# Kernel optimization log

Measured on AMD Instinct MI355X. Metric: run time of the kernel, lower is better.

Reference implementation:

```python
import jax, jax.numpy as jnp
import numpy as np

B_SZ, IN_DIM, N_NEURONS, N_LAYERS, N_OUTS = 65536, 4, 512, 8, 4


def setup_inputs() -> dict:
    key = jax.random.key(0)
    ks = jax.random.split(key, 5)
    glorot = lambda k, shape: jax.random.normal(k, shape, jnp.float32) * np.sqrt(2.0 / (shape[-2] + shape[-1]))
    inputs = jax.random.normal(ks[0], (B_SZ, IN_DIM), jnp.float32)
    # GaussianRFF projection matrix (fixed random Gaussian)
    B_rff = jax.random.normal(ks[1], (IN_DIM, N_NEURONS // 2), jnp.float32)
    Ws = glorot(ks[2], (N_LAYERS, N_NEURONS, N_NEURONS))
    bs = jnp.zeros((N_LAYERS, N_NEURONS), jnp.float32)
    alphas = jnp.zeros((N_LAYERS + 1,), jnp.float32)  # LAAF slopes, init 0
    Wf = glorot(ks[3], (N_NEURONS, N_OUTS))           # final mixer, no bias
    scale = jnp.ones((N_OUTS,), jnp.float32)          # Scaler, no bias
    return {"inputs": inputs, "B_rff": B_rff, "Ws": Ws, "bs": bs,
            "alphas": alphas, "Wf": Wf, "scale": scale}


def _mlp(x, B_rff, Ws, bs, alphas, Wf, scale):
    # Gaussian random Fourier feature embedding -> [B, n_neurons]
    z = x @ B_rff
    u = jnp.concatenate([jnp.sin(z), jnp.cos(z)], axis=-1)
    L = Ws.shape[0]
    def step(u, p):
        W, b, a = p
        # LAAF sine layer: sin(w0 * (1 + alpha) * (uW + b)), w0 = 1.0
        return jnp.sin((1.0 + a) * (u @ W + b)), None
    u, _ = jax.lax.scan(step, u, (Ws, bs, alphas[:L]))
    return (u @ Wf) * scale  # [B, 4] = (A1, A2, A3, phi)


def reference(inputs, B_rff, Ws, bs, alphas, Wf, scale):
    f = lambda x: _mlp(x, B_rff, Ws, bs, alphas, Wf, scale)
    def jvp_col(col):
        tang = jnp.zeros_like(inputs).at[:, col].set(1.0)
        return jax.jvp(f, (inputs,), (tang,))
    # input columns: 0=t, 1=z, 2=x, 3=y
    P, dPdz = jvp_col(1)
    _, dPdx = jvp_col(2)
    _, dPdy = jvp_col(3)
    A1_y, A1_z = dPdy[:, 0:1], dPdz[:, 0:1]
    A2_x, A2_z = dPdx[:, 1:2], dPdz[:, 1:2]
    A3_x, A3_y = dPdx[:, 2:3], dPdy[:, 2:3]
    phi_x, phi_y, phi_z = dPdx[:, 3:4], dPdy[:, 3:4], dPdz[:, 3:4]
    u = (A3_y - A2_z) + phi_x
    v = (A1_z - A3_x) + phi_y
    w = (A2_x - A1_y) + phi_z
    return jnp.concatenate([u, v, w], axis=1)
```

## Files before the change

### kernel.cpp

```cpp
#include <hip/hip_runtime.h>
#include <stdint.h>


#define B_SZ   65536
#define NN     512
#define NL     8
#define SPB    24
#define MROWS  96
#define MT     6
#define NTW    4
#define NKB    16
#define KB_BYTES 32768
#define LDS_A  (MROWS*1024)
#define LDS_TOTAL (LDS_A + 2*KB_BYTES)

typedef _Float16 f16x8 __attribute__((ext_vector_type(8)));
typedef float    f32x4 __attribute__((ext_vector_type(4)));

__device__ __forceinline__ uint16_t f2h_bits(float f) {
  union { _Float16 h; uint16_t u; } v; v.h = (_Float16)f; return v.u;
}
__device__ __forceinline__ float h2f(uint16_t b) {
  union { uint16_t u; _Float16 h; } v; v.u = b; return (float)v.h;
}

__global__ __launch_bounds__(512) void prep_weights(const float* __restrict__ Ws,
                                                    uint16_t* __restrict__ img) {
  const int n  = threadIdx.x;
  const int kb = blockIdx.x & 15;
  const int l  = blockIdx.x >> 4;
  const float* src = Ws + ((size_t)l << 18) + n;
  char* dstbase = (char*)img + (((size_t)(l*16 + kb)) << 15) + (size_t)n * 64;
  #pragma unroll
  for (int kq = 0; kq < 4; ++kq) {
    uint16_t h[8];
    #pragma unroll
    for (int e = 0; e < 8; ++e) {
      int k = kb*32 + kq*8 + e;
      h[e] = f2h_bits(src[(size_t)k * 512]);
    }
    uint4 pk;
    pk.x = (uint32_t)h[0] | ((uint32_t)h[1] << 16);
    pk.y = (uint32_t)h[2] | ((uint32_t)h[3] << 16);
    pk.z = (uint32_t)h[4] | ((uint32_t)h[5] << 16);
    pk.w = (uint32_t)h[6] | ((uint32_t)h[7] << 16);
    *(uint4*)(dstbase + 16 * ((kq + (n >> 1)) & 3)) = pk;
  }
}

__global__ __launch_bounds__(512, 2) void pinn_fused(
    const float* __restrict__ inputs, const float* __restrict__ Brff,
    const float* __restrict__ bs, const float* __restrict__ alphas,
    const float* __restrict__ Wf, const float* __restrict__ scl,
    const uint16_t* __restrict__ wimg, float* __restrict__ out)
{
  extern __shared__ char smem[];
  char* wbuf0 = smem + LDS_A;
  char* wbuf1 = smem + LDS_A + KB_BYTES;

  const int tid  = threadIdx.x;
  const int lane = tid & 63;
  const int wv   = tid >> 6;
  const int i16  = lane & 15;
  const int q    = lane >> 4;
  const int sbase = blockIdx.x * SPB;

  float* brff = (float*)wbuf0;
  brff[tid]       = Brff[tid];
  brff[tid + 512] = Brff[tid + 512];
  __syncthreads();

  {
    const int k = tid;
    const int col = k & 255;
    const bool iscos = (k >= 256);
    const float b0 = brff[col], b1 = brff[256 + col], b2 = brff[512 + col], b3 = brff[768 + col];
    for (int m = 0; m < MROWS; ++m) {
      int s = sbase + (m >> 2); if (s >= B_SZ) s = B_SZ - 1;
      const int stream = m & 3;
      const float* x = inputs + (size_t)s * 4;
      float z = x[0]*b0 + x[1]*b1 + x[2]*b2 + x[3]*b3;
      float szn = __sinf(z), czn = __cosf(z);
      float val;
      if (stream == 0) val = iscos ? czn : szn;
      else {
        float bc = (stream == 1) ? b1 : (stream == 2 ? b2 : b3);
        val = iscos ? (-szn * bc) : (czn * bc);
      }
      *(uint16_t*)(smem + m*1024 + ((2*k) ^ ((m & 7) * 16))) = f2h_bits(val);
    }
  }
  __syncthreads();

  auto stage = [&](int g, char* buf) {
    const char* src = (const char*)wimg + ((size_t)g << 15) + (size_t)(wv*4) * 1024 + (size_t)lane * 16;
    char* dst = buf + (wv*4) * 1024;
    #pragma unroll
    for (int it = 0; it < 4; ++it) {
      __builtin_amdgcn_global_load_lds(
          (const __attribute__((address_space(1))) void*)(src + it*1024),
          (__attribute__((address_space(3))) void*)(dst + it*1024),
          16, 0, 0);
    }
  };

  stage(0, wbuf0);
  __syncthreads();

  f32x4 acc[MT][NTW];

  for (int l = 0; l < NL; ++l) {
    const f32x4 zz = {0.f, 0.f, 0.f, 0.f};
    #pragma unroll
    for (int a = 0; a < MT; ++a)
      #pragma unroll
      for (int b = 0; b < NTW; ++b)
        acc[a][b] = zz;

    for (int kb = 0; kb < NKB; ++kb) {
      const int g = l*NKB + kb;
      char* cur = (g & 1) ? wbuf1 : wbuf0;
      if (g + 1 < NL*NKB) stage(g + 1, (g & 1) ? wbuf0 : wbuf1);

      f16x8 af[MT];
      #pragma unroll
      for (int Mt = 0; Mt < MT; ++Mt) {
        const int m = Mt*16 + i16;
        af[Mt] = *(const f16x8*)(smem + m*1024 + ((kb*64 + q*16) ^ ((i16 & 7) * 16)));
      }
      f16x8 bfr[NTW];
      #pragma unroll
      for (int Nt = 0; Nt < NTW; ++Nt) {
        const int nc = wv*64 + Nt*16 + i16;
        bfr[Nt] = *(const f16x8*)(cur + nc*64 + 16 * ((q + (nc >> 1)) & 3));
      }
      #pragma unroll
      for (int Mt = 0; Mt < MT; ++Mt)
        #pragma unroll
        for (int Nt = 0; Nt < NTW; ++Nt)
          acc[Mt][Nt] = __builtin_amdgcn_mfma_f32_16x16x32_f16(af[Mt], bfr[Nt], acc[Mt][Nt], 0, 0, 0);
      __syncthreads();
    }

    const float opa = 1.0f + alphas[l];
    #pragma unroll
    for (int Nt = 0; Nt < NTW; ++Nt) {
      const int nc = wv*64 + Nt*16 + i16;
      const float bias = bs[l*NN + nc];
      #pragma unroll
      for (int Mt = 0; Mt < MT; ++Mt) {
        f32x4 c = acc[Mt][Nt];
        float h  = opa * (c[0] + bias);
        float un = __sinf(h);
        float fc = opa * __cosf(h);
        float vv[4] = { un, fc*c[1], fc*c[2], fc*c[3] };
        const int mb = Mt*16 + q*4;
        #pragma unroll
        for (int r = 0; r < 4; ++r) {
          const int m = mb + r;
          *(uint16_t*)(smem + m*1024 + ((2*nc) ^ ((m & 7) * 16))) = f2h_bits(vv[r]);
        }
      }
    }
    __syncthreads();
  }

  float* dp = (float*)wbuf0;
  const float4 sc4 = *(const float4*)scl;
  for (int rr = 0; rr < MROWS/8; ++rr) {
    const int m = wv * 12 + rr;
    float p0 = 0.f, p1 = 0.f, p2 = 0.f, p3 = 0.f;
    #pragma unroll
    for (int j = 0; j < 8; ++j) {
      const int k = lane + j*64;
      float a = h2f(*(const uint16_t*)(smem + m*1024 + ((2*k) ^ ((m & 7) * 16))));
      float4 wf = ((const float4*)Wf)[k];
      p0 += a*wf.x; p1 += a*wf.y; p2 += a*wf.z; p3 += a*wf.w;
    }
    #pragma unroll
    for (int d = 1; d < 64; d <<= 1) {
      p0 += __shfl_xor(p0, d, 64);
      p1 += __shfl_xor(p1, d, 64);
      p2 += __shfl_xor(p2, d, 64);
      p3 += __shfl_xor(p3, d, 64);
    }
    if (lane == 0) {
      float4* o = (float4*)(dp + m*4);
      *o = make_float4(p0*sc4.x, p1*sc4.y, p2*sc4.z, p3*sc4.w);
    }
  }
  __syncthreads();

  if (tid < SPB*3) {
    const int sl = tid / 3, c = tid - sl*3;
    const int s = sbase + sl;
    if (s < B_SZ) {
      const float* d1 = dp + (sl*4 + 1)*4;
      const float* d2 = dp + (sl*4 + 2)*4;
      const float* d3 = dp + (sl*4 + 3)*4;
      float val;
      if (c == 0)      val = d3[2] - d1[1] + d2[3];
      else if (c == 1) val = d1[0] - d2[2] + d3[3];
      else             val = d2[1] - d3[0] + d1[3];
      out[(size_t)s*3 + c] = val;
    }
  }
}

extern "C" void kernel_launch(void* const* d_in, const int* in_sizes, int n_in,
                              void* d_out, int out_size, void* d_ws, size_t ws_size,
                              hipStream_t stream) {
  const float* inputs = (const float*)d_in[0];
  const float* Brff   = (const float*)d_in[1];
  const float* Ws     = (const float*)d_in[2];
  const float* bsp    = (const float*)d_in[3];
  const float* alph   = (const float*)d_in[4];
  const float* Wfp    = (const float*)d_in[5];
  const float* sclp   = (const float*)d_in[6];
  uint16_t* wimg = (uint16_t*)d_ws;

  prep_weights<<<NL*NKB/2 * 2 , 512, 0, stream>>>(Ws, wimg);
  const int nblocks = (B_SZ + SPB - 1) / SPB;
  pinn_fused<<<nblocks, 512, LDS_TOTAL, stream>>>(inputs, Brff, bsp, alph, Wfp, sclp,
                                                  wimg, (float*)d_out);
}
```

Measured before the change: 1.433 ms.

## Load weight fragments directly from global into registers, drop LDS weight staging

Replaces the double-buffered global-to-LDS staging of each 32KB weight k-block with direct per-lane global loads of B fragments into registers, prefetched one k-block ahead. This removes the per-k-block __syncthreads and cuts LDS use from about 160KB to about 100KB, which may allow more resident blocks. In exchange, each wave now reads its weight fragments from L2/global with less latency hiding than the LDS pipeline gave, and global weight traffic per block rises because no data is shared through LDS.

```diff
diff --git a/kernel.cpp b/kernel.cpp
--- a/kernel.cpp
+++ b/kernel.cpp
@@ -10,9 +10,9 @@
 #define MT     6
 #define NTW    4
 #define NKB    16
-#define KB_BYTES 32768
 #define LDS_A  (MROWS*1024)
-#define LDS_TOTAL (LDS_A + 2*KB_BYTES)
+#define LDS_AUX 4096
+#define LDS_TOTAL (LDS_A + LDS_AUX)
 
 typedef _Float16 f16x8 __attribute__((ext_vector_type(8)));
 typedef float    f32x4 __attribute__((ext_vector_type(4)));
@@ -55,8 +55,7 @@
     const uint16_t* __restrict__ wimg, float* __restrict__ out)
 {
   extern __shared__ char smem[];
-  char* wbuf0 = smem + LDS_A;
-  char* wbuf1 = smem + LDS_A + KB_BYTES;
+  char* aux = smem + LDS_A;
 
   const int tid  = threadIdx.x;
   const int lane = tid & 63;
@@ -65,7 +64,7 @@
   const int q    = lane >> 4;
   const int sbase = blockIdx.x * SPB;
 
-  float* brff = (float*)wbuf0;
+  float* brff = (float*)aux;
   brff[tid]       = Brff[tid];
   brff[tid + 512] = Brff[tid + 512];
   __syncthreads();
@@ -92,24 +91,18 @@
   }
   __syncthreads();
 
-  auto stage = [&](int g, char* buf) {
-    const char* src = (const char*)wimg + ((size_t)g << 15) + (size_t)(wv*4) * 1024 + (size_t)lane * 16;
-    char* dst = buf + (wv*4) * 1024;
-    #pragma unroll
-    for (int it = 0; it < 4; ++it) {
-      __builtin_amdgcn_global_load_lds(
-          (const __attribute__((address_space(1))) void*)(src + it*1024),
-          (__attribute__((address_space(3))) void*)(dst + it*1024),
-          16, 0, 0);
-    }
-  };
-
-  stage(0, wbuf0);
-  __syncthreads();
+  int boff[NTW];
+  #pragma unroll
+  for (int Nt = 0; Nt < NTW; ++Nt) {
+    const int nc = wv*64 + Nt*16 + i16;
+    boff[Nt] = nc*64 + 16 * ((q + (nc >> 1)) & 3);
+  }
 
   f32x4 acc[MT][NTW];
 
   for (int l = 0; l < NL; ++l) {
+    const char* wl = (const char*)wimg + ((size_t)l << 19);
+
     const f32x4 zz = {0.f, 0.f, 0.f, 0.f};
     #pragma unroll
     for (int a = 0; a < MT; ++a)
@@ -117,30 +110,28 @@
       for (int b = 0; b < NTW; ++b)
         acc[a][b] = zz;
 
+    f16x8 bfr[2][NTW];
+    #pragma unroll
+    for (int Nt = 0; Nt < NTW; ++Nt)
+      bfr[0][Nt] = *(const f16x8*)(wl + boff[Nt]);
+
     for (int kb = 0; kb < NKB; ++kb) {
-      const int g = l*NKB + kb;
-      char* cur = (g & 1) ? wbuf1 : wbuf0;
-      if (g + 1 < NL*NKB) stage(g + 1, (g & 1) ? wbuf0 : wbuf1);
-
-      f16x8 af[MT];
+      if (kb + 1 < NKB) {
+        const char* bn = wl + (size_t)(kb + 1) * 32768;
+        #pragma unroll
+        for (int Nt = 0; Nt < NTW; ++Nt)
+          bfr[(kb + 1) & 1][Nt] = *(const f16x8*)(bn + boff[Nt]);
+      }
+      const int koff = (kb*64 + q*16) ^ ((i16 & 7) * 16);
       #pragma unroll
       for (int Mt = 0; Mt < MT; ++Mt) {
-        const int m = Mt*16 + i16;
-        af[Mt] = *(const f16x8*)(smem + m*1024 + ((kb*64 + q*16) ^ ((i16 & 7) * 16)));
-      }
-      f16x8 bfr[NTW];
-      #pragma unroll
-      for (int Nt = 0; Nt < NTW; ++Nt) {
-        const int nc = wv*64 + Nt*16 + i16;
-        bfr[Nt] = *(const f16x8*)(cur + nc*64 + 16 * ((q + (nc >> 1)) & 3));
-      }
-      #pragma unroll
-      for (int Mt = 0; Mt < MT; ++Mt)
+        const f16x8 af = *(const f16x8*)(smem + (Mt*16 + i16)*1024 + koff);
         #pragma unroll
         for (int Nt = 0; Nt < NTW; ++Nt)
-          acc[Mt][Nt] = __builtin_amdgcn_mfma_f32_16x16x32_f16(af[Mt], bfr[Nt], acc[Mt][Nt], 0, 0, 0);
-      __syncthreads();
-    }
+          acc[Mt][Nt] = __builtin_amdgcn_mfma_f32_16x16x32_f16(af, bfr[kb & 1][Nt], acc[Mt][Nt], 0, 0, 0);
+      }
+    }
+    __syncthreads();
 
     const float opa = 1.0f + alphas[l];
     #pragma unroll
@@ -165,7 +156,7 @@
     __syncthreads();
   }
 
-  float* dp = (float*)wbuf0;
+  float* dp = (float*)aux;
   const float4 sc4 = *(const float4*)scl;
   for (int rr = 0; rr < MROWS/8; ++rr) {
     const int m = wv * 12 + rr;
@@ -219,7 +210,7 @@
   const float* sclp   = (const float*)d_in[6];
   uint16_t* wimg = (uint16_t*)d_ws;
 
-  prep_weights<<<NL*NKB/2 * 2 , 512, 0, stream>>>(Ws, wimg);
+  prep_weights<<<NL*NKB, 512, 0, stream>>>(Ws, wimg);
   const int nblocks = (B_SZ + SPB - 1) / SPB;
   pinn_fused<<<nblocks, 512, LDS_TOTAL, stream>>>(inputs, Brff, bsp, alph, Wfp, sclp,
                                                   wimg, (float*)d_out);
```

Measured after the change: 2.530 ms. 1.77x slower.
